# Optimization experiments

Hardware: AMD Instinct MI355X
Metric: run time of the kernel (lower is better)

The kernel has to match this reference:

```python
import jax, jax.numpy as jnp
import numpy as np

HEADS = 16
DIM_HEAD = 64
SCALE = DIM_HEAD ** -0.5


def setup_inputs() -> dict:
    key = jax.random.key(0)
    k1, k2, k3 = jax.random.split(key, 3)
    B, N, D = 8, 1024, 1024
    x = jax.random.normal(k1, (B, N, D), dtype=jnp.float32)
    # 0/1 keep-mask over the N-1 non-prepended positions
    mask = jax.random.randint(k2, (B, N - 1), 0, 2, dtype=jnp.int32)
    # Linear(dim, 3*inner_dim, bias=False); stored as [dim, 3*inner] so y = x @ W
    w_qkv = jax.random.normal(k3, (D, 3 * HEADS * DIM_HEAD), dtype=jnp.float32) * (D ** -0.5)
    return {"x": x, "mask": mask, "w_qkv": w_qkv}


def reference(x, mask, w_qkv):
    b, n, _ = x.shape
    h, d = HEADS, DIM_HEAD
    qkv = x @ w_qkv                                    # [b, n, 3*h*d]
    q, k, v = jnp.split(qkv, 3, axis=-1)
    to_heads = lambda t: t.reshape(b, n, h, d).transpose(0, 2, 1, 3)  # b h n d
    q, k, v = to_heads(q), to_heads(k), to_heads(v)
    dots = jnp.einsum('bhid,bhjd->bhij', q, k) * SCALE  # [b, h, n, n]
    # F.pad(mask.flatten(1), (1,0), value=1.0) -> prepend a kept position
    m = jnp.pad(mask.reshape(b, -1).astype(jnp.float32), ((0, 0), (1, 0)),
                constant_values=1.0)                    # [b, n]
    dots = dots - 10000.0 * (1.0 - m)[:, None, None, :]
    attn = jax.nn.softmax(dots, axis=-1)
    out = jnp.einsum('bhij,bhjd->bhid', attn, v)        # [b, h, n, d]
    return out.transpose(0, 2, 1, 3).reshape(b, n, h * d)
```

## Files before the change

kernel.cpp:

```cpp
#include <hip/hip_runtime.h>
#include <hip/hip_bf16.h>
#include <stdint.h>

#define HEADS 16
#define DH    64
#define SEQ   1024
#define DIM   1024

typedef __attribute__((ext_vector_type(8))) short bf16x8;
typedef __attribute__((ext_vector_type(4))) float f32x4;
typedef __attribute__((ext_vector_type(16))) float f32x16;
typedef __attribute__((ext_vector_type(4))) unsigned int u32x4;

#define QSCALE_L2 0.18033688011112042f
#define THR_L2 11.541560327111707f
#define PEN_L2 (-14427.0f)

static __device__ __forceinline__ unsigned short f2bf(float f) {
  unsigned u = __builtin_bit_cast(unsigned, f);
  u += 0x7fff + ((u >> 16) & 1);
  return (unsigned short)(u >> 16);
}

static __device__ __forceinline__ float fexp2(float x) {
#if __has_builtin(__builtin_amdgcn_exp2f)
  return __builtin_amdgcn_exp2f(x);
#else
  return exp2f(x);
#endif
}

static __device__ __forceinline__ void gload_lds16(const void* g, void* l) {
  __builtin_amdgcn_global_load_lds(
      (const __attribute__((address_space(1))) unsigned int*)g,
      (__attribute__((address_space(3))) unsigned int*)l,
      16, 0, 0);
}

__global__ __launch_bounds__(256) void build_keep(
    const int* __restrict__ mask, int* __restrict__ inv, int* __restrict__ nkeep) {
  const int b = blockIdx.x;
  const int t = threadIdx.x;
  __shared__ int sc[256];
  int kept[4];
  int c = 0;
#pragma unroll
  for (int k = 0; k < 4; ++k) {
    const int j = t * 4 + k;
    const int kp = (j == 0) ? 1 : (mask[b * (SEQ - 1) + j - 1] != 0);
    kept[k] = kp;
    c += kp;
  }
  sc[t] = c;
  __syncthreads();
  for (int off = 1; off < 256; off <<= 1) {
    const int v = (t >= off) ? sc[t - off] : 0;
    __syncthreads();
    sc[t] += v;
    __syncthreads();
  }
  int pos = sc[t] - c;
  const int total = sc[255];
#pragma unroll
  for (int k = 0; k < 4; ++k) {
    const int j = t * 4 + k;
    inv[b * SEQ + j] = kept[k] ? pos : -1;
    pos += kept[k];
  }
  if (t == 0) nkeep[b] = total;
}

__global__ __launch_bounds__(256) void cvt_x(
    const float* __restrict__ in, unsigned short* __restrict__ out) {
  const int i = (blockIdx.x * 256 + threadIdx.x) * 4;
  const float4 v = *reinterpret_cast<const float4*>(in + i);
  short4 o;
  o.x = (short)f2bf(v.x);
  o.y = (short)f2bf(v.y);
  o.z = (short)f2bf(v.z);
  o.w = (short)f2bf(v.w);
  *reinterpret_cast<short4*>(out + i) = o;
}

__global__ __launch_bounds__(256) void transpose_w(
    const float* __restrict__ w, unsigned short* __restrict__ wT) {
  __shared__ unsigned short t[64][68];
  const int tid = threadIdx.x;
  const int bk = blockIdx.x;
  const int bn = blockIdx.y;
  const int r = tid >> 4;
  const int c = (tid & 15) * 4;
#pragma unroll
  for (int rr = 0; rr < 64; rr += 16) {
    const float4 v = *reinterpret_cast<const float4*>(
        w + (size_t)(bk * 64 + r + rr) * 3072 + bn * 64 + c);
    t[r + rr][c + 0] = f2bf(v.x);
    t[r + rr][c + 1] = f2bf(v.y);
    t[r + rr][c + 2] = f2bf(v.z);
    t[r + rr][c + 3] = f2bf(v.w);
  }
  __syncthreads();
#pragma unroll
  for (int rr = 0; rr < 64; rr += 16) {
    short4 o;
    o.x = (short)t[c + 0][r + rr];
    o.y = (short)t[c + 1][r + rr];
    o.z = (short)t[c + 2][r + rr];
    o.w = (short)t[c + 3][r + rr];
    *reinterpret_cast<short4*>(
        wT + (size_t)(bn * 64 + r + rr) * 1024 + bk * 64 + c) = o;
  }
}

__global__ __launch_bounds__(256) void qkv_gemm(
    const unsigned short* __restrict__ x, const unsigned short* __restrict__ wT,
    const int* __restrict__ inv,
    unsigned short* __restrict__ Qh, unsigned short* __restrict__ Kc,
    unsigned short* __restrict__ Vc) {
  __shared__ unsigned short Al[128 * 32];
  __shared__ unsigned short Bl[128 * 32];
  const int tid = threadIdx.x;
  const int lane = tid & 63;
  const int wave = tid >> 6;
  const int m0 = blockIdx.x * 128;
  const int n0 = blockIdx.y * 128;
  const int wm = (wave >> 1) * 64;
  const int wn = (wave & 1) * 64;
  const int l15 = lane & 15;
  const int kb8 = (lane >> 4) * 8;
  const int lg4 = (lane >> 4) * 4;

  f32x4 acc[4][4] = {};

  for (int kt = 0; kt < DIM; kt += 32) {
    __syncthreads();
#pragma unroll
    for (int rnd = 0; rnd < 2; ++rnd) {
      const int off = tid * 16 + rnd * 4096;
      const int row = off >> 6;
      const int kc = (off & 63) >> 1;
      gload_lds16(x + (size_t)(m0 + row) * DIM + kt + kc, (char*)Al + off);
      gload_lds16(wT + (size_t)(n0 + row) * DIM + kt + kc, (char*)Bl + off);
    }
    __syncthreads();
    bf16x8 af[4], bfr[4];
#pragma unroll
    for (int i = 0; i < 4; ++i)
      af[i] = *reinterpret_cast<const bf16x8*>(&Al[(wm + i * 16 + l15) * 32 + kb8]);
#pragma unroll
    for (int j = 0; j < 4; ++j)
      bfr[j] = *reinterpret_cast<const bf16x8*>(&Bl[(wn + j * 16 + l15) * 32 + kb8]);
#pragma unroll
    for (int i = 0; i < 4; ++i)
#pragma unroll
      for (int j = 0; j < 4; ++j)
        acc[i][j] = __builtin_amdgcn_mfma_f32_16x16x32_bf16(af[i], bfr[j], acc[i][j], 0, 0, 0);
  }

  __syncthreads();
  unsigned short* Sw = (wave < 2 ? Al : Bl) + (wave & 1) * (16 * 72);
  const int sec = n0 >> 10;
  const float sc = (sec == 0) ? QSCALE_L2 : 1.0f;
  const int h = ((n0 + wn) >> 6) & 15;
#pragma unroll
  for (int i = 0; i < 4; ++i) {
#pragma unroll
    for (int j = 0; j < 4; ++j)
#pragma unroll
      for (int r = 0; r < 4; ++r)
        Sw[(lg4 + r) * 72 + j * 16 + l15] = f2bf(acc[i][j][r] * sc);
#pragma unroll
    for (int pass = 0; pass < 2; ++pass) {
      const int row = pass * 8 + (lane >> 3);
      const int chunk = lane & 7;
      const bf16x8 vv = *reinterpret_cast<const bf16x8*>(&Sw[row * 72 + chunk * 8]);
      const int grow = m0 + wm + i * 16 + row;
      const int b = grow >> 10;
      const int n = grow & 1023;
      const size_t bh = (size_t)b * HEADS + h;
      if (sec == 0) {
        *reinterpret_cast<bf16x8*>(&Qh[(bh * SEQ + n) * DH + chunk * 8]) = vv;
      } else {
        const int iv = inv[b * SEQ + n];
        if (iv >= 0) {
          if (sec == 1)
            *reinterpret_cast<bf16x8*>(&Kc[(bh * SEQ + iv) * DH + chunk * 8]) = vv;
          else
            *reinterpret_cast<bf16x8*>(&Vc[(bh * SEQ + iv) * DH + chunk * 8]) = vv;
        }
      }
    }
  }
}

__global__ __launch_bounds__(256) void transpose_v(
    const unsigned short* __restrict__ Vc, unsigned short* __restrict__ Vtc) {
  __shared__ unsigned short t[64][72];
  const int tid = threadIdx.x;
  const int i0 = blockIdx.x * 64;
  const int bhi = blockIdx.y;
  const unsigned short* src = Vc + (size_t)bhi * SEQ * DH;
  unsigned short* dst = Vtc + (size_t)bhi * DH * SEQ;
  const int r = tid >> 3;
  const int c = (tid & 7) * 8;
#pragma unroll
  for (int rr = 0; rr < 64; rr += 32) {
    const bf16x8 v = *reinterpret_cast<const bf16x8*>(
        src + (size_t)(i0 + r + rr) * DH + c);
    *reinterpret_cast<bf16x8*>(&t[r + rr][c]) = v;
  }
  __syncthreads();
#pragma unroll
  for (int dd = 0; dd < 64; dd += 32) {
    const int d = r + dd;
    bf16x8 o;
#pragma unroll
    for (int e = 0; e < 8; ++e) o[e] = (short)t[c + e][d];
    *reinterpret_cast<bf16x8*>(dst + (size_t)d * SEQ + i0 + c) = o;
  }
}

__global__ __launch_bounds__(256) void attn_fwd5(
    const unsigned short* __restrict__ Qh, const unsigned short* __restrict__ Kc,
    const unsigned short* __restrict__ Vtc,
    const int* __restrict__ nkeep, float* __restrict__ out) {
  __shared__ alignas(16) unsigned char Kl[2][8192];
  __shared__ alignas(16) unsigned char Vl[2][8192];
  __shared__ float corrw[4][32];
  const int tid = threadIdx.x;
  const int lane = tid & 63;
  const int wave = tid >> 6;
  const int l31 = lane & 31;
  const int hi = lane >> 5;
  const int h8 = hi * 8;
  const bool islo = lane < 32;

  const int bid = ((blockIdx.x & 7) << 7) | (blockIdx.x >> 3);
  const int b = bid >> 7;
  const int hh = (bid >> 3) & 15;
  const int qc = bid & 7;
  const size_t bh = (size_t)b * HEADS + hh;
  const int q0 = qc * 128 + wave * 32;

  const int nk = nkeep[b];
  const int ntile = (nk + 63) >> 6;

  const unsigned short* Q = Qh + bh * SEQ * DH;
  const unsigned short* K = Kc + bh * SEQ * DH;
  const unsigned short* V = Vtc + bh * DH * SEQ;

  auto STAGE = [&](int buf, int kt) {
#pragma unroll
    for (int p = 0; p < 2; ++p) {
      const int off = p * 4096 + tid * 16;
      const int row = off >> 7;
      const int chunk = (off >> 4) & 7;
      const int sch = chunk ^ (row & 7);
      gload_lds16(K + (size_t)(kt + row) * DH + sch * 8, &Kl[buf][off]);
      gload_lds16(V + (size_t)row * SEQ + kt + sch * 8, &Vl[buf][off]);
    }
  };

  STAGE(0, 0);

  bf16x8 qf[4];
#pragma unroll
  for (int ds = 0; ds < 4; ++ds)
    qf[ds] = *reinterpret_cast<const bf16x8*>(
        Q + (size_t)(q0 + l31) * DH + ds * 16 + h8);

  u32x4 onesu = {0u, 0u, 0u, 0u};
  onesu.x = islo ? 0x3F80u : 0u;
  const bf16x8 onesf = __builtin_bit_cast(bf16x8, onesu);

  f32x16 Od0 = (f32x16)0.f, Od1 = (f32x16)0.f;
  float m_ = 0.f, l_ = 0.f;

  __syncthreads();

  int cur = 0;
  for (int ti = 0; ti < ntile; ++ti) {
    const int kt = ti * 64;
    if (ti + 1 < ntile) STAGE(cur ^ 1, kt + 64);

    f32x16 st0 = (f32x16)0.f, st1 = (f32x16)0.f;
    __builtin_amdgcn_s_setprio(1);
#pragma unroll
    for (int ds = 0; ds < 4; ++ds) {
      const int c0 = (ds * 2 + hi) ^ (l31 & 7);
      const bf16x8 kf0 = *reinterpret_cast<const bf16x8*>(
          &Kl[cur][l31 * 128 + c0 * 16]);
      st0 = __builtin_amdgcn_mfma_f32_32x32x16_bf16(kf0, qf[ds], st0, 0, 0, 0);
      const bf16x8 kf1 = *reinterpret_cast<const bf16x8*>(
          &Kl[cur][(32 + l31) * 128 + c0 * 16]);
      st1 = __builtin_amdgcn_mfma_f32_32x32x16_bf16(kf1, qf[ds], st1, 0, 0, 0);
    }
    __builtin_amdgcn_s_setprio(0);

    if (ti == ntile - 1) {
      const unsigned short pv = f2bf(PEN_L2);
      const unsigned short pu0 = (kt + l31 < nk) ? (unsigned short)0 : pv;
      const unsigned short pu1 = (kt + 32 + l31 < nk) ? (unsigned short)0 : pv;
      u32x4 p0 = {0u, 0u, 0u, 0u}, p1 = {0u, 0u, 0u, 0u};
      p0.x = islo ? (unsigned)pu0 : 0u;
      p1.x = islo ? (unsigned)pu1 : 0u;
      st0 = __builtin_amdgcn_mfma_f32_32x32x16_bf16(
          __builtin_bit_cast(bf16x8, p0), onesf, st0, 0, 0, 0);
      st1 = __builtin_amdgcn_mfma_f32_32x32x16_bf16(
          __builtin_bit_cast(bf16x8, p1), onesf, st1, 0, 0, 0);
    }
    float a[8];
#pragma unroll
    for (int i = 0; i < 8; ++i)
      a[i] = fmaxf(fmaxf(st0[i], st0[i + 8]), fmaxf(st1[i], st1[i + 8]));
#pragma unroll
    for (int k = 4; k >= 1; k >>= 1)
#pragma unroll
      for (int i = 0; i < k; ++i) a[i] = fmaxf(a[i], a[i + k]);
    const float mx = fmaxf(a[0], __shfl_xor(a[0], 32));
    if (!__all(mx <= m_ + THR_L2)) {
      const float mn = fmaxf(m_, mx);
      const float corr = fexp2(m_ - mn);
      m_ = mn;
      l_ *= corr;
      if (islo) corrw[wave][l31] = corr;
      f32x4 cv[4];
#pragma unroll
      for (int j = 0; j < 4; ++j)
        cv[j] = *reinterpret_cast<const f32x4*>(&corrw[wave][j * 8 + (h8 >> 1)]);
#pragma unroll
      for (int r = 0; r < 16; ++r) {
        Od0[r] *= cv[r >> 2][r & 3];
        Od1[r] *= cv[r >> 2][r & 3];
      }
    }
#pragma unroll
    for (int i = 0; i < 16; ++i) {
      st0[i] = fexp2(st0[i] - m_);
      st1[i] = fexp2(st1[i] - m_);
    }
    float s8[8];
#pragma unroll
    for (int i = 0; i < 8; ++i)
      s8[i] = (st0[i] + st0[i + 8]) + (st1[i] + st1[i + 8]);
#pragma unroll
    for (int k = 4; k >= 1; k >>= 1)
#pragma unroll
      for (int i = 0; i < k; ++i) s8[i] += s8[i + k];
    l_ += s8[0] + __shfl_xor(s8[0], 32);
    bf16x8 pf[4];
#pragma unroll
    for (int t = 0; t < 2; ++t) {
#pragma unroll
      for (int bq = 0; bq < 2; ++bq) {
        const int o = 8 * bq;
        float e0 = t ? st1[o + 0] : st0[o + 0], e1 = t ? st1[o + 1] : st0[o + 1];
        float e2 = t ? st1[o + 2] : st0[o + 2], e3 = t ? st1[o + 3] : st0[o + 3];
        float e4 = t ? st1[o + 4] : st0[o + 4], e5 = t ? st1[o + 5] : st0[o + 5];
        float e6 = t ? st1[o + 6] : st0[o + 6], e7 = t ? st1[o + 7] : st0[o + 7];
        unsigned A0, A1, B0, B1;
        asm("v_cvt_pk_bf16_f32 %0, %1, %2" : "=v"(A0) : "v"(e0), "v"(e1));
        asm("v_cvt_pk_bf16_f32 %0, %1, %2" : "=v"(A1) : "v"(e2), "v"(e3));
        asm("v_cvt_pk_bf16_f32 %0, %1, %2" : "=v"(B0) : "v"(e4), "v"(e5));
        asm("v_cvt_pk_bf16_f32 %0, %1, %2" : "=v"(B1) : "v"(e6), "v"(e7));
        asm("v_permlane32_swap_b32 %0, %1\n\ts_nop 1" : "+v"(A0), "+v"(B0));
        asm("v_permlane32_swap_b32 %0, %1\n\ts_nop 1" : "+v"(A1), "+v"(B1));
        u32x4 pk4;
        pk4.x = A0; pk4.y = A1; pk4.z = B0; pk4.w = B1;
        pf[t * 2 + bq] = __builtin_bit_cast(bf16x8, pk4);
      }
    }
    __builtin_amdgcn_s_setprio(1);
#pragma unroll
    for (int kvs = 0; kvs < 4; ++kvs) {
      const int c0 = (kvs * 2 + hi) ^ (l31 & 7);
      const bf16x8 v0 = *reinterpret_cast<const bf16x8*>(
          &Vl[cur][l31 * 128 + c0 * 16]);
      Od0 = __builtin_amdgcn_mfma_f32_32x32x16_bf16(pf[kvs], v0, Od0, 0, 0, 0);
      const bf16x8 v1 = *reinterpret_cast<const bf16x8*>(
          &Vl[cur][(32 + l31) * 128 + c0 * 16]);
      Od1 = __builtin_amdgcn_mfma_f32_32x32x16_bf16(pf[kvs], v1, Od1, 0, 0, 0);
    }
    __builtin_amdgcn_s_setprio(0);

    __syncthreads();
    cur ^= 1;
  }

  if (islo) corrw[wave][l31] = 1.0f / l_;
  f32x4 lv[4];
#pragma unroll
  for (int j = 0; j < 4; ++j)
    lv[j] = *reinterpret_cast<const f32x4*>(&corrw[wave][j * 8 + (h8 >> 1)]);
#pragma unroll
  for (int r = 0; r < 16; ++r) {
    const int q = q0 + (r & 3) + 8 * (r >> 2) + (hi << 2);
    out[((size_t)b * SEQ + q) * (HEADS * DH) + hh * DH + 0 * 32 + l31] =
        Od0[r] * lv[r >> 2][r & 3];
    out[((size_t)b * SEQ + q) * (HEADS * DH) + hh * DH + 1 * 32 + l31] =
        Od1[r] * lv[r >> 2][r & 3];
  }
}

extern "C" void kernel_launch(void* const* d_in, const int* in_sizes, int n_in,
                              void* d_out, int out_size, void* d_ws, size_t ws_size,
                              hipStream_t stream) {
  const float* x = (const float*)d_in[0];
  const int* mask = (const int*)d_in[1];
  const float* w = (const float*)d_in[2];
  float* outp = (float*)d_out;

  char* ws = (char*)d_ws;
  unsigned short* xb   = (unsigned short*)(ws);
  unsigned short* wT   = (unsigned short*)(ws + 16777216);
  unsigned short* Qh   = (unsigned short*)(ws + 23068672);
  unsigned short* Kc   = (unsigned short*)(ws + 39845888);
  unsigned short* Vc   = (unsigned short*)(ws + 56623104);
  int*            inv  = (int*)(ws + 73400320);
  int*            nkp  = (int*)(ws + 73433088);
  unsigned short* Vtc  = xb;

  build_keep<<<dim3(8), 256, 0, stream>>>(mask, inv, nkp);
  cvt_x<<<dim3(8192), 256, 0, stream>>>(x, xb);
  transpose_w<<<dim3(16, 48), 256, 0, stream>>>(w, wT);
  qkv_gemm<<<dim3(64, 24), 256, 0, stream>>>(xb, wT, inv, Qh, Kc, Vc);
  transpose_v<<<dim3(16, 128), 256, 0, stream>>>(Vc, Vtc);
  attn_fwd5<<<dim3(1024), 256, 0, stream>>>(Qh, Kc, Vtc, nkp, outp);
}
```

Baseline: 131.7 us.

## Double-buffer QKV GEMM LDS tiles with XOR swizzle and wider K step

Rewrites the QKV projection GEMM main loop to double-buffer A/B tiles in LDS, issuing the next tile's global-to-LDS loads before computing on the current one and waiting with partial vmcnt. The K step grows from 32 to 64 and LDS rows are XOR-swizzled to avoid bank conflicts on fragment reads. This is meant to hide global load latency and cut sync overhead, at the cost of four times the LDS use (64KB per block), which may lower occupancy.

```diff
diff --git a/kernel.cpp b/kernel.cpp
--- a/kernel.cpp
+++ b/kernel.cpp
@@ -117,8 +117,7 @@
     const int* __restrict__ inv,
     unsigned short* __restrict__ Qh, unsigned short* __restrict__ Kc,
     unsigned short* __restrict__ Vc) {
-  __shared__ unsigned short Al[128 * 32];
-  __shared__ unsigned short Bl[128 * 32];
+  __shared__ alignas(16) unsigned char L[2][2][16384];
   const int tid = threadIdx.x;
   const int lane = tid & 63;
   const int wave = tid >> 6;
@@ -127,38 +126,62 @@
   const int wm = (wave >> 1) * 64;
   const int wn = (wave & 1) * 64;
   const int l15 = lane & 15;
-  const int kb8 = (lane >> 4) * 8;
-  const int lg4 = (lane >> 4) * 4;
+  const int lg = lane >> 4;
+  const int lg4 = lg * 4;
 
   f32x4 acc[4][4] = {};
 
-  for (int kt = 0; kt < DIM; kt += 32) {
-    __syncthreads();
-#pragma unroll
-    for (int rnd = 0; rnd < 2; ++rnd) {
-      const int off = tid * 16 + rnd * 4096;
-      const int row = off >> 6;
-      const int kc = (off & 63) >> 1;
-      gload_lds16(x + (size_t)(m0 + row) * DIM + kt + kc, (char*)Al + off);
-      gload_lds16(wT + (size_t)(n0 + row) * DIM + kt + kc, (char*)Bl + off);
-    }
-    __syncthreads();
-    bf16x8 af[4], bfr[4];
-#pragma unroll
-    for (int i = 0; i < 4; ++i)
-      af[i] = *reinterpret_cast<const bf16x8*>(&Al[(wm + i * 16 + l15) * 32 + kb8]);
-#pragma unroll
-    for (int j = 0; j < 4; ++j)
-      bfr[j] = *reinterpret_cast<const bf16x8*>(&Bl[(wn + j * 16 + l15) * 32 + kb8]);
-#pragma unroll
-    for (int i = 0; i < 4; ++i)
-#pragma unroll
-      for (int j = 0; j < 4; ++j)
-        acc[i][j] = __builtin_amdgcn_mfma_f32_16x16x32_bf16(af[i], bfr[j], acc[i][j], 0, 0, 0);
-  }
-
-  __syncthreads();
-  unsigned short* Sw = (wave < 2 ? Al : Bl) + (wave & 1) * (16 * 72);
+  auto STAGE = [&](int buf, int kt) {
+#pragma unroll
+    for (int r = 0; r < 4; ++r) {
+      const int o = r * 4096 + tid * 16;
+      const int row = o >> 7;
+      const int sch = ((o >> 4) & 7) ^ (row & 7);
+      gload_lds16(x + (size_t)(m0 + row) * DIM + kt + sch * 8, &L[buf][0][o]);
+      gload_lds16(wT + (size_t)(n0 + row) * DIM + kt + sch * 8, &L[buf][1][o]);
+    }
+  };
+
+  STAGE(0, 0);
+
+  for (int t = 0; t < 16; ++t) {
+    const int kt = t * 64;
+    if (t < 15) {
+      STAGE((t + 1) & 1, kt + 64);
+      asm volatile("s_waitcnt vmcnt(8)" ::: "memory");
+    } else {
+      asm volatile("s_waitcnt vmcnt(0)" ::: "memory");
+    }
+    __builtin_amdgcn_s_barrier();
+
+    const unsigned char* Abuf = &L[t & 1][0][0];
+    const unsigned char* Bbuf = &L[t & 1][1][0];
+    bf16x8 af[4][2], bfr[4][2];
+#pragma unroll
+    for (int i = 0; i < 4; ++i) {
+#pragma unroll
+      for (int kk = 0; kk < 2; ++kk) {
+        const int ra = wm + i * 16 + l15;
+        af[i][kk] = *reinterpret_cast<const bf16x8*>(
+            Abuf + ra * 128 + (((kk * 4 + lg) ^ (ra & 7)) << 4));
+        const int rb = wn + i * 16 + l15;
+        bfr[i][kk] = *reinterpret_cast<const bf16x8*>(
+            Bbuf + rb * 128 + (((kk * 4 + lg) ^ (rb & 7)) << 4));
+      }
+    }
+#pragma unroll
+    for (int kk = 0; kk < 2; ++kk)
+#pragma unroll
+      for (int i = 0; i < 4; ++i)
+#pragma unroll
+        for (int j = 0; j < 4; ++j)
+          acc[i][j] = __builtin_amdgcn_mfma_f32_16x16x32_bf16(
+              af[i][kk], bfr[j][kk], acc[i][j], 0, 0, 0);
+
+    __builtin_amdgcn_s_barrier();
+  }
+
+  unsigned short* Sw = reinterpret_cast<unsigned short*>(&L[0][0][0] + wave * 2304);
   const int sec = n0 >> 10;
   const float sc = (sec == 0) ? QSCALE_L2 : 1.0f;
   const int h = ((n0 + wn) >> 6) & 15;
```

New measurement: 134.8 us. +2.3%, slower.
